# Performance work log

Hardware: AMD Instinct MI355X
Metric: run time of the kernel (lower is better)

The kernel has to match this reference:

```python
import jax, jax.numpy as jnp
import numpy as np

SCALE_DIM = 64  # output_size, used as 1/sqrt(d) scale per source code


def setup_inputs() -> dict:
    key = jax.random.key(0)
    ks = jax.random.split(key, 6)
    B, S, D_IN, D_OUT = 4, 4096, 512, 64
    return {
        "key_inputs": jax.random.normal(ks[0], (B, S, D_IN), dtype=jnp.float32),
        "value_inputs": jax.random.normal(ks[1], (B, S, D_IN), dtype=jnp.float32),
        "query_inputs": jax.random.normal(ks[2], (B, S, D_IN), dtype=jnp.float32),
        "Wq": jax.random.normal(ks[3], (D_IN, D_OUT), dtype=jnp.float32) * 0.05,
        "Wk": jax.random.normal(ks[4], (D_IN, D_OUT), dtype=jnp.float32) * 0.05,
        "Wv": jax.random.normal(ks[5], (D_IN, D_OUT), dtype=jnp.float32) * 0.05,
    }


def reference(key_inputs, value_inputs, query_inputs, Wq, Wk, Wv):
    # QKV projections: [B,S,D_in] x [D_in,D_out] -> [B,S,D_out]
    Q = jnp.einsum("bsd,de->bse", query_inputs, Wq)
    K = jnp.einsum("bsd,de->bse", key_inputs, Wk)
    V = jnp.einsum("bsd,de->bse", value_inputs, Wv)
    d = K.shape[2]
    # scores: [B, Sq, Sk]
    scores = jnp.einsum("bqe,bke->bqk", Q, K) / jnp.sqrt(jnp.float32(d))
    # causal mask: strictly-upper-triangular -inf (source: transpose(tril(-inf, -1)))
    Sq, Sk = Q.shape[1], K.shape[1]
    causal = jnp.tril(jnp.ones((Sq, Sk), dtype=bool))
    scores = jnp.where(causal[None, :, :], scores, -jnp.inf)
    attn = jax.nn.softmax(scores, axis=-1)
    Z = jnp.einsum("bqk,bke->bqe", attn, V)
    return Z
```

## Files before the change

kernel.cpp:

```cpp
#include <hip/hip_runtime.h>
#include <hip/hip_bf16.h>

#define BATCH 4
#define SEQ   4096
#define DIN   512
#define DOUT  64

typedef __attribute__((ext_vector_type(4))) float f32x4;
typedef __attribute__((ext_vector_type(8))) short bf16x8;
typedef __attribute__((ext_vector_type(4))) short bf16x4;

__device__ __forceinline__ f32x4 mfma16(bf16x8 a, bf16x8 b, f32x4 c) {
    return __builtin_amdgcn_mfma_f32_16x16x32_bf16(a, b, c, 0, 0, 0);
}
__device__ __forceinline__ f32x4 mfma16k(bf16x4 a, bf16x4 b, f32x4 c) {
    return __builtin_amdgcn_mfma_f32_16x16x16bf16_1k(a, b, c, 0, 0, 0);
}

__device__ __forceinline__ short f2bf(float f) {
    union { float f; unsigned u; } x; x.f = f;
    unsigned r = x.u + 0x7FFFu + ((x.u >> 16) & 1u);
    return (short)(r >> 16);
}

__device__ __forceinline__ unsigned pack_bf2(float lo, float hi) {
    union { float f; unsigned u; } a, b; a.f = lo; b.f = hi;
    return __builtin_amdgcn_perm(b.u, a.u, 0x07060302u);
}

__device__ __forceinline__ void dma16(const void* g, void* l) {
    __builtin_amdgcn_global_load_lds(
        (const __attribute__((address_space(1))) void*)g,
        (__attribute__((address_space(3))) void*)l, 16, 0, 0);
}

#define QSCALE 0.1803368801111204f

__global__ __launch_bounds__(256) void wconv_kernel(
    const float* __restrict__ Wq, const float* __restrict__ Wk,
    const float* __restrict__ Wv, short* __restrict__ Wt)
{
    const int m = blockIdx.y;
    const float* W = (m == 0) ? Wq : (m == 1) ? Wk : Wv;
    const int idx = blockIdx.x * 256 + threadIdx.x;
    const int k = idx >> 6;
    const int n = idx & 63;
    Wt[m * (DOUT * DIN) + n * DIN + k] = f2bf(W[idx]);
}

__global__ __launch_bounds__(256) void proj_kernel(
    const float* __restrict__ Xq, const float* __restrict__ Xk, const float* __restrict__ Xv,
    const short* __restrict__ Wt,
    short* __restrict__ Qb, short* __restrict__ Kb, short* __restrict__ Vt)
{
    __shared__ __align__(16) char smem[2][24576];

    const int m = blockIdx.y;
    const float* X  = (m == 0) ? Xq : (m == 1) ? Xk : Xv;
    const short* Wm = Wt + m * (DOUT * DIN);

    const int tid  = threadIdx.x;
    const int wv   = tid >> 6;
    const int lane = tid & 63;
    const int quad = lane >> 4;
    const int l16  = lane & 15;
    const long waveRow = (long)blockIdx.x * 64 + wv * 16;

    const float* xg = X  + (waveRow + l16) * DIN + quad * 8;
    const short* wg = Wm + (long)(wv * 16 + l16) * DIN + quad * 8;

    f32x4 acc[4];
    #pragma unroll
    for (int e = 0; e < 4; ++e) acc[e] = (f32x4){0.f, 0.f, 0.f, 0.f};

#define STAGE_PROJ(B) do {                                   \
        char* xb_ = &smem[(B)][0] + wv * 4096;               \
        char* wb_ = &smem[(B)][0] + 16384 + wv * 2048;       \
        dma16(xg,      xb_);                                 \
        dma16(xg + 4,  xb_ + 1024);                          \
        dma16(xg + 32, xb_ + 2048);                          \
        dma16(xg + 36, xb_ + 3072);                          \
        dma16(wg,      wb_);                                 \
        dma16(wg + 32, wb_ + 1024);                          \
    } while (0)

    STAGE_PROJ(0);
    xg += 64; wg += 64;
    __syncthreads();

    for (int kt = 0; kt < 8; ++kt) {
        const int cur = kt & 1;
        if (kt < 7) {
            if (cur) { STAGE_PROJ(0); } else { STAGE_PROJ(1); }
            xg += 64; wg += 64;
        }
        const char* xb = &smem[cur][0] + wv * 4096;
        const char* wb = &smem[cur][0] + 16384;
        #pragma unroll
        for (int c2 = 0; c2 < 2; ++c2) {
            float4 xa = *(const float4*)(xb + c2 * 2048 + lane * 16);
            float4 xc = *(const float4*)(xb + c2 * 2048 + 1024 + lane * 16);
            bf16x8 af;
            af[0] = f2bf(xa.x); af[1] = f2bf(xa.y); af[2] = f2bf(xa.z); af[3] = f2bf(xa.w);
            af[4] = f2bf(xc.x); af[5] = f2bf(xc.y); af[6] = f2bf(xc.z); af[7] = f2bf(xc.w);
            #pragma unroll
            for (int e = 0; e < 4; ++e) {
                bf16x8 bf = *(const bf16x8*)(wb + (e * 2 + c2) * 1024 + lane * 16);
                if (m < 2) acc[e] = mfma16(af, bf, acc[e]);
                else       acc[e] = mfma16(bf, af, acc[e]);
            }
        }
        __syncthreads();
    }
#undef STAGE_PROJ

    if (m < 2) {
        short* O = (m == 0) ? Qb : Kb;
        const float sc = (m == 0) ? QSCALE : 1.0f;
        #pragma unroll
        for (int e = 0; e < 4; ++e)
            #pragma unroll
            for (int r = 0; r < 4; ++r)
                O[(waveRow + quad * 4 + r) * DOUT + e * 16 + l16] = f2bf(acc[e][r] * sc);
    } else {
        const long b = waveRow >> 12;
        const long s = waveRow & (SEQ - 1);
        #pragma unroll
        for (int e = 0; e < 4; ++e)
            #pragma unroll
            for (int r = 0; r < 4; ++r)
                Vt[(b * DOUT + e * 16 + quad * 4 + r) * SEQ + s + l16] = f2bf(acc[e][r]);
    }
}

__global__ __launch_bounds__(256) void flash_kernel(
    const short* __restrict__ Qb, const short* __restrict__ Kb,
    const short* __restrict__ Vt, float* __restrict__ Out)
{
    __shared__ __align__(16) char smem[65536];

    const int i    = blockIdx.x;
    const int b    = (i & 7) >> 1;
    const int qt   = 255 - (((i >> 3) << 1) | (i & 1));
    const int tid  = threadIdx.x;
    const int wv   = tid >> 6;
    const int lane = tid & 63;
    const int quad = lane >> 4;
    const int l16  = lane & 15;
    const int q0   = qt * 16;

    const short* Qp = Qb + ((long)b * SEQ + q0 + l16) * DOUT + quad * 8;
    bf16x8 qf0 = *(const bf16x8*)(Qp);
    bf16x8 qf1 = *(const bf16x8*)(Qp + 32);

    const short* Kbase  = Kb + (long)b * SEQ * DOUT;
    const short* VbaseG = Vt + (long)b * DOUT * SEQ;

    const short* gk = Kbase + (long)(wv * 64 + l16) * DOUT + quad * 8;
    const short* gv = VbaseG + (long)(lane >> 3) * SEQ + wv * 64
                    + (((lane & 7) ^ ((lane >> 3) & 7)) * 8);

    char* ks = smem + wv * 8192;
    char* vs = smem + 32768 + wv * 8192;

    f32x4 acc[4];
    #pragma unroll
    for (int e = 0; e < 4; ++e) acc[e] = (f32x4){0.f, 0.f, 0.f, 0.f};
    float mrow = -1e30f, lrow = 0.f;

    const int q_hi  = q0 + 15;
    const int qg    = q0 + l16;
    const int wbase = wv * 64;
    const int R     = q0 / 256 + 1;
    const int f8    = (l16 & 7) << 1;

    for (int r = 0; r < R; ++r) {
        const int kv0 = r * 256;
        const bool act = (kv0 + wbase) <= q_hi;

        if (act) {
            dma16(gk,                  ks);
            dma16(gk + 32,             ks + 1024);
            dma16(gk + 16 * DOUT,      ks + 2048);
            dma16(gk + 16 * DOUT + 32, ks + 3072);
            dma16(gk + 32 * DOUT,      ks + 4096);
            dma16(gk + 32 * DOUT + 32, ks + 5120);
            dma16(gk + 48 * DOUT,      ks + 6144);
            dma16(gk + 48 * DOUT + 32, ks + 7168);
            dma16(gv,           vs);
            dma16(gv +  8 * SEQ, vs + 1024);
            dma16(gv + 16 * SEQ, vs + 2048);
            dma16(gv + 24 * SEQ, vs + 3072);
            dma16(gv + 32 * SEQ, vs + 4096);
            dma16(gv + 40 * SEQ, vs + 5120);
            dma16(gv + 48 * SEQ, vs + 6144);
            dma16(gv + 56 * SEQ, vs + 7168);
        }
        __syncthreads();

        if (act) {
            f32x4 sc[4];
            #pragma unroll
            for (int kh = 0; kh < 4; ++kh) {
                bf16x8 k0 = *(const bf16x8*)(ks + (kh * 2 + 0) * 1024 + lane * 16);
                bf16x8 k1 = *(const bf16x8*)(ks + (kh * 2 + 1) * 1024 + lane * 16);
                f32x4 z = (f32x4){0.f, 0.f, 0.f, 0.f};
                z = mfma16(k0, qf0, z);
                z = mfma16(k1, qf1, z);
                sc[kh] = z;
            }

            #pragma unroll
            for (int kh = 0; kh < 4; ++kh)
                #pragma unroll
                for (int rr = 0; rr < 4; ++rr)
                    sc[kh][rr] = ((kv0 + wbase + kh * 16 + quad * 4 + rr) <= qg)
                               ? sc[kh][rr] : -1e30f;

            float tm = -1e30f;
            #pragma unroll
            for (int kh = 0; kh < 4; ++kh)
                #pragma unroll
                for (int rr = 0; rr < 4; ++rr) tm = fmaxf(tm, sc[kh][rr]);
            tm = fmaxf(tm, __shfl_xor(tm, 16, 64));
            tm = fmaxf(tm, __shfl_xor(tm, 32, 64));
            const float mn = fmaxf(mrow, tm);
            const float alpha = __builtin_amdgcn_exp2f(mrow - mn);
            mrow = mn;
            float p[4][4];
            float rs = 0.f;
            #pragma unroll
            for (int kh = 0; kh < 4; ++kh)
                #pragma unroll
                for (int rr = 0; rr < 4; ++rr) {
                    p[kh][rr] = __builtin_amdgcn_exp2f(sc[kh][rr] - mn);
                    rs += p[kh][rr];
                }
            rs += __shfl_xor(rs, 16, 64);
            rs += __shfl_xor(rs, 32, 64);
            lrow = lrow * alpha + rs;
            #pragma unroll
            for (int e = 0; e < 4; ++e)
                #pragma unroll
                for (int rr = 0; rr < 4; ++rr) acc[e][rr] *= alpha;

            union { unsigned u[2]; bf16x4 v; } pf[4];
            #pragma unroll
            for (int kh = 0; kh < 4; ++kh) {
                pf[kh].u[0] = pack_bf2(p[kh][0], p[kh][1]);
                pf[kh].u[1] = pack_bf2(p[kh][2], p[kh][3]);
            }

            #pragma unroll
            for (int kh = 0; kh < 4; ++kh) {
                #pragma unroll
                for (int et = 0; et < 4; ++et) {
                    const int e = et * 16 + l16;
                    const int g = kh * 4 + quad;
                    bf16x4 cv = *(const bf16x4*)(vs + e * 128 + ((g ^ f8) * 8));
                    acc[et] = mfma16k(cv, pf[kh].v, acc[et]);
                }
            }
        }
        __syncthreads();

        gk += 256 * DOUT;
        gv += 256;
    }

    float* s_m   = (float*)smem;
    float* s_l   = (float*)(smem + 256);
    float* s_acc = (float*)(smem + 512);

    if (quad == 0) { s_m[wv * 16 + l16] = mrow; s_l[wv * 16 + l16] = lrow; }
    #pragma unroll
    for (int et = 0; et < 4; ++et)
        #pragma unroll
        for (int rr = 0; rr < 4; ++rr)
            s_acc[(wv * 16 + l16) * 65 + et * 16 + quad * 4 + rr] = acc[et][rr];
    __syncthreads();

    const int col = tid & 63;
    const int r0  = (tid >> 6) * 4;
    float* outp = Out + ((long)b * SEQ + q0) * DOUT;
    #pragma unroll
    for (int rr = 0; rr < 4; ++rr) {
        const int row = r0 + rr;
        const float m0 = s_m[row], m1 = s_m[16 + row];
        const float m2 = s_m[32 + row], m3 = s_m[48 + row];
        const float mM = fmaxf(fmaxf(m0, m1), fmaxf(m2, m3));
        const float a0 = __builtin_amdgcn_exp2f(m0 - mM);
        const float a1 = __builtin_amdgcn_exp2f(m1 - mM);
        const float a2 = __builtin_amdgcn_exp2f(m2 - mM);
        const float a3 = __builtin_amdgcn_exp2f(m3 - mM);
        const float li = a0 * s_l[row] + a1 * s_l[16 + row]
                       + a2 * s_l[32 + row] + a3 * s_l[48 + row];
        const float o  = a0 * s_acc[(0 * 16 + row) * 65 + col]
                       + a1 * s_acc[(1 * 16 + row) * 65 + col]
                       + a2 * s_acc[(2 * 16 + row) * 65 + col]
                       + a3 * s_acc[(3 * 16 + row) * 65 + col];
        outp[row * DOUT + col] = o / li;
    }
}

extern "C" void kernel_launch(void* const* d_in, const int* in_sizes, int n_in,
                              void* d_out, int out_size, void* d_ws, size_t ws_size,
                              hipStream_t stream) {
    const float* key_in   = (const float*)d_in[0];
    const float* value_in = (const float*)d_in[1];
    const float* query_in = (const float*)d_in[2];
    const float* Wq = (const float*)d_in[3];
    const float* Wk = (const float*)d_in[4];
    const float* Wv = (const float*)d_in[5];
    float* out = (float*)d_out;

    short* Qb = (short*)d_ws;
    short* Kb = Qb + (long)BATCH * SEQ * DOUT;
    short* Vt = Kb + (long)BATCH * SEQ * DOUT;
    short* Wt = Vt + (long)BATCH * SEQ * DOUT;

    dim3 wgrid((DOUT * DIN) / 256, 3);
    wconv_kernel<<<wgrid, 256, 0, stream>>>(Wq, Wk, Wv, Wt);

    dim3 pgrid(BATCH * SEQ / 64, 3);
    proj_kernel<<<pgrid, 256, 0, stream>>>(query_in, key_in, value_in,
                                           Wt, Qb, Kb, Vt);

    flash_kernel<<<dim3(SEQ / 16 * BATCH), 256, 0, stream>>>(Qb, Kb, Vt, out);
}
```

Before: 181.7 us.

## Double-buffer K/V tiles and process 32 query rows per block

Each block now handles 32 query rows, split across two wave pairs, and each pair splits a 128-key tile in halves. K/V staging is double-buffered, so the next tile's async copies are issued before computing on the current one, hiding load latency and halving the per-block K/V traffic per query. The trade-off is fewer blocks (512), more rounds per block with smaller tiles, and a new swizzle for the V layout.

After: 178.0 us. 2.0% less time.

```diff
diff --git a/kernel.cpp b/kernel.cpp
--- a/kernel.cpp
+++ b/kernel.cpp
@@ -137,73 +137,75 @@
     const short* __restrict__ Qb, const short* __restrict__ Kb,
     const short* __restrict__ Vt, float* __restrict__ Out)
 {
-    __shared__ __align__(16) char smem[65536];
+    __shared__ __align__(16) char smem[2][32768];
 
     const int i    = blockIdx.x;
     const int b    = (i & 7) >> 1;
-    const int qt   = 255 - (((i >> 3) << 1) | (i & 1));
+    const int t    = 127 - (((i >> 3) << 1) | (i & 1));
     const int tid  = threadIdx.x;
     const int wv   = tid >> 6;
     const int lane = tid & 63;
     const int quad = lane >> 4;
     const int l16  = lane & 15;
-    const int q0   = qt * 16;
-
-    const short* Qp = Qb + ((long)b * SEQ + q0 + l16) * DOUT + quad * 8;
+    const int wq   = wv >> 1;
+    const int wk   = wv & 1;
+    const int q0w  = t * 32 + wq * 16;
+
+    const short* Qp = Qb + ((long)b * SEQ + q0w + l16) * DOUT + quad * 8;
     bf16x8 qf0 = *(const bf16x8*)(Qp);
     bf16x8 qf1 = *(const bf16x8*)(Qp + 32);
 
     const short* Kbase  = Kb + (long)b * SEQ * DOUT;
     const short* VbaseG = Vt + (long)b * DOUT * SEQ;
 
-    const short* gk = Kbase + (long)(wv * 64 + l16) * DOUT + quad * 8;
-    const short* gv = VbaseG + (long)(lane >> 3) * SEQ + wv * 64
-                    + (((lane & 7) ^ ((lane >> 3) & 7)) * 8);
-
-    char* ks = smem + wv * 8192;
-    char* vs = smem + 32768 + wv * 8192;
+    const short* gk = Kbase + (long)(wv * 16 + l16) * DOUT + quad * 8;
+    const int erow = 4 * wv + (lane >> 4);
+    const int cgr  = (lane & 15) ^ (erow & 15);
+    const short* gv = VbaseG + (long)erow * SEQ + cgr * 8;
 
     f32x4 acc[4];
     #pragma unroll
     for (int e = 0; e < 4; ++e) acc[e] = (f32x4){0.f, 0.f, 0.f, 0.f};
     float mrow = -1e30f, lrow = 0.f;
 
-    const int q_hi  = q0 + 15;
-    const int qg    = q0 + l16;
-    const int wbase = wv * 64;
-    const int R     = q0 / 256 + 1;
-    const int f8    = (l16 & 7) << 1;
+    const int q_hi   = q0w + 15;
+    const int qg     = q0w + l16;
+    const int wfirst = wk * 64;
+    const int R      = t / 4 + 1;
+
+#define STAGE_KV(B, KV0) do {                                         \
+        char* kb_ = &smem[(B)][0];                                    \
+        char* vb_ = &smem[(B)][0] + 16384;                            \
+        const short* gkp_ = gk + (long)(KV0) * DOUT;                  \
+        dma16(gkp_,                  kb_ + (2 * wv) * 1024);          \
+        dma16(gkp_ + 32,             kb_ + (2 * wv + 1) * 1024);      \
+        dma16(gkp_ + 64 * DOUT,      kb_ + (2 * wv + 8) * 1024);      \
+        dma16(gkp_ + 64 * DOUT + 32, kb_ + (2 * wv + 9) * 1024);      \
+        const short* gvp_ = gv + (KV0);                               \
+        dma16(gvp_,            vb_ + (wv)      * 1024);               \
+        dma16(gvp_ + 16 * SEQ, vb_ + (wv + 4)  * 1024);               \
+        dma16(gvp_ + 32 * SEQ, vb_ + (wv + 8)  * 1024);               \
+        dma16(gvp_ + 48 * SEQ, vb_ + (wv + 12) * 1024);               \
+    } while (0)
+
+    STAGE_KV(0, 0);
+    __syncthreads();
 
     for (int r = 0; r < R; ++r) {
-        const int kv0 = r * 256;
-        const bool act = (kv0 + wbase) <= q_hi;
-
-        if (act) {
-            dma16(gk,                  ks);
-            dma16(gk + 32,             ks + 1024);
-            dma16(gk + 16 * DOUT,      ks + 2048);
-            dma16(gk + 16 * DOUT + 32, ks + 3072);
-            dma16(gk + 32 * DOUT,      ks + 4096);
-            dma16(gk + 32 * DOUT + 32, ks + 5120);
-            dma16(gk + 48 * DOUT,      ks + 6144);
-            dma16(gk + 48 * DOUT + 32, ks + 7168);
-            dma16(gv,           vs);
-            dma16(gv +  8 * SEQ, vs + 1024);
-            dma16(gv + 16 * SEQ, vs + 2048);
-            dma16(gv + 24 * SEQ, vs + 3072);
-            dma16(gv + 32 * SEQ, vs + 4096);
-            dma16(gv + 40 * SEQ, vs + 5120);
-            dma16(gv + 48 * SEQ, vs + 6144);
-            dma16(gv + 56 * SEQ, vs + 7168);
-        }
-        __syncthreads();
-
-        if (act) {
+        const int kv0 = r * 128;
+        const int cur = r & 1;
+        if (r + 1 < R) STAGE_KV(cur ^ 1, kv0 + 128);
+
+        if ((kv0 + wfirst) <= q_hi) {
+            const char* kb = &smem[cur][0];
+            const char* vb = &smem[cur][0] + 16384;
+
             f32x4 sc[4];
             #pragma unroll
             for (int kh = 0; kh < 4; ++kh) {
-                bf16x8 k0 = *(const bf16x8*)(ks + (kh * 2 + 0) * 1024 + lane * 16);
-                bf16x8 k1 = *(const bf16x8*)(ks + (kh * 2 + 1) * 1024 + lane * 16);
+                const int slot = (wk * 4 + kh) * 2;
+                bf16x8 k0 = *(const bf16x8*)(kb + slot * 1024 + lane * 16);
+                bf16x8 k1 = *(const bf16x8*)(kb + (slot + 1) * 1024 + lane * 16);
                 f32x4 z = (f32x4){0.f, 0.f, 0.f, 0.f};
                 z = mfma16(k0, qf0, z);
                 z = mfma16(k1, qf1, z);
@@ -214,7 +216,7 @@
             for (int kh = 0; kh < 4; ++kh)
                 #pragma unroll
                 for (int rr = 0; rr < 4; ++rr)
-                    sc[kh][rr] = ((kv0 + wbase + kh * 16 + quad * 4 + rr) <= qg)
+                    sc[kh][rr] = ((kv0 + wfirst + kh * 16 + quad * 4 + rr) <= qg)
                                ? sc[kh][rr] : -1e30f;
 
             float tm = -1e30f;
@@ -253,24 +255,23 @@
 
             #pragma unroll
             for (int kh = 0; kh < 4; ++kh) {
+                const int gbase = wk * 8 + kh * 2 + (quad >> 1);
                 #pragma unroll
                 for (int et = 0; et < 4; ++et) {
                     const int e = et * 16 + l16;
-                    const int g = kh * 4 + quad;
-                    bf16x4 cv = *(const bf16x4*)(vs + e * 128 + ((g ^ f8) * 8));
+                    bf16x4 cv = *(const bf16x4*)(vb + e * 256
+                                   + ((gbase ^ (e & 15)) * 16) + (quad & 1) * 8);
                     acc[et] = mfma16k(cv, pf[kh].v, acc[et]);
                 }
             }
         }
         __syncthreads();
-
-        gk += 256 * DOUT;
-        gv += 256;
     }
-
-    float* s_m   = (float*)smem;
-    float* s_l   = (float*)(smem + 256);
-    float* s_acc = (float*)(smem + 512);
+#undef STAGE_KV
+
+    float* s_m   = (float*)&smem[0][0];
+    float* s_l   = s_m + 64;
+    float* s_acc = s_l + 64;
 
     if (quad == 0) { s_m[wv * 16 + l16] = mrow; s_l[wv * 16 + l16] = lrow; }
     #pragma unroll
@@ -280,25 +281,21 @@
             s_acc[(wv * 16 + l16) * 65 + et * 16 + quad * 4 + rr] = acc[et][rr];
     __syncthreads();
 
-    const int col = tid & 63;
-    const int r0  = (tid >> 6) * 4;
-    float* outp = Out + ((long)b * SEQ + q0) * DOUT;
+    const int col   = tid & 63;
+    const int rbase = (tid >> 6) * 8;
+    float* outp = Out + ((long)b * SEQ + t * 32) * DOUT;
     #pragma unroll
-    for (int rr = 0; rr < 4; ++rr) {
-        const int row = r0 + rr;
-        const float m0 = s_m[row], m1 = s_m[16 + row];
-        const float m2 = s_m[32 + row], m3 = s_m[48 + row];
-        const float mM = fmaxf(fmaxf(m0, m1), fmaxf(m2, m3));
+    for (int k = 0; k < 8; ++k) {
+        const int row = rbase + k;
+        const int w0  = (row >> 4) * 2;
+        const int lr  = row & 15;
+        const float m0 = s_m[w0 * 16 + lr], m1 = s_m[(w0 + 1) * 16 + lr];
+        const float mM = fmaxf(m0, m1);
         const float a0 = __builtin_amdgcn_exp2f(m0 - mM);
         const float a1 = __builtin_amdgcn_exp2f(m1 - mM);
-        const float a2 = __builtin_amdgcn_exp2f(m2 - mM);
-        const float a3 = __builtin_amdgcn_exp2f(m3 - mM);
-        const float li = a0 * s_l[row] + a1 * s_l[16 + row]
-                       + a2 * s_l[32 + row] + a3 * s_l[48 + row];
-        const float o  = a0 * s_acc[(0 * 16 + row) * 65 + col]
-                       + a1 * s_acc[(1 * 16 + row) * 65 + col]
-                       + a2 * s_acc[(2 * 16 + row) * 65 + col]
-                       + a3 * s_acc[(3 * 16 + row) * 65 + col];
+        const float li = a0 * s_l[w0 * 16 + lr] + a1 * s_l[(w0 + 1) * 16 + lr];
+        const float o  = a0 * s_acc[(w0 * 16 + lr) * 65 + col]
+                       + a1 * s_acc[((w0 + 1) * 16 + lr) * 65 + col];
         outp[row * DOUT + col] = o / li;
     }
 }
@@ -326,5 +323,5 @@
     proj_kernel<<<pgrid, 256, 0, stream>>>(query_in, key_in, value_in,
                                            Wt, Qb, Kb, Vt);
 
-    flash_kernel<<<dim3(SEQ / 16 * BATCH), 256, 0, stream>>>(Qb, Kb, Vt, out);
-}
+    flash_kernel<<<dim3(SEQ / 32 * BATCH), 256, 0, stream>>>(Qb, Kb, Vt, out);
+}
```
